# Optimization experiments

Hardware: AMD Instinct MI355X
Metric: run time of the kernel (lower is better)

Reference implementation:

```python
import jax, jax.numpy as jnp
import numpy as np

N_NODES = 50000


def gcn_conv(x, edge_index, W, b):
    """PyG GCNConv: h = x @ W; add self-loops; symmetric deg^-1/2 norm; scatter-add; + bias."""
    h = x @ W                                   # [N, C_out]
    n = x.shape[0]
    loops = jnp.arange(n, dtype=edge_index.dtype)
    src = jnp.concatenate([edge_index[0], loops])   # [E + N]
    dst = jnp.concatenate([edge_index[1], loops])   # [E + N]
    deg = jax.ops.segment_sum(jnp.ones_like(src, dtype=h.dtype), dst, num_segments=n)
    dinv = jnp.where(deg > 0, jax.lax.rsqrt(deg), 0.0)
    norm = dinv[src] * dinv[dst]                # [E + N]
    msg = h[src] * norm[:, None]                # gather + edgewise scale
    out = jax.ops.segment_sum(msg, dst, num_segments=n)  # scatter-add
    return out + b


def setup_inputs() -> dict:
    key = jax.random.key(0)
    k1, k2, k3, k4 = jax.random.split(key, 4)
    x = jax.random.normal(k1, (N_NODES, 128), dtype=jnp.float32)
    edge_index = jax.random.randint(k2, (2, 800000), 0, N_NODES, dtype=jnp.int32)
    W1 = jax.random.normal(k3, (128, 128), dtype=jnp.float32) * (1.0 / np.sqrt(128))
    b1 = jnp.zeros((128,), dtype=jnp.float32)
    W2 = jax.random.normal(k4, (128, 64), dtype=jnp.float32) * (1.0 / np.sqrt(128))
    b2 = jnp.zeros((64,), dtype=jnp.float32)
    return {"x": x, "edge_index": edge_index, "W1": W1, "b1": b1, "W2": W2, "b2": b2}


def reference(x, edge_index, W1, b1, W2, b2):
    h = gcn_conv(x, edge_index, W1, b1)
    h = jax.nn.relu(h)
    out = gcn_conv(h, edge_index, W2, b2)
    return out
```

## Files before the change

kernel.cpp:

```cpp
#include <hip/hip_runtime.h>
#include <hip/hip_bf16.h>
#include <math.h>

#define N_NODES 50000
#define N_EDGES 800000
#define NSLICE 8
#define SLICE_NODES 6400
#define CSR_W 48
#define EDGE_CHUNKS ((N_EDGES + 1023) / 1024)
#define GROUPS 196

typedef unsigned int uint;
typedef unsigned short ushort;
typedef __attribute__((ext_vector_type(8))) short bf16x8;
typedef __attribute__((ext_vector_type(4))) float f32x4;

__device__ __forceinline__ float bf16_lo(uint u) { return __uint_as_float(u << 16); }
__device__ __forceinline__ float bf16_hi(uint u) { return __uint_as_float(u & 0xFFFF0000u); }
__device__ __forceinline__ ushort f2bf(float a) {
    return __bfloat16_as_ushort(__float2bfloat16(a));
}
__device__ __forceinline__ uint pack_bf2(float a, float b) {
    return ((uint)f2bf(b) << 16) | (uint)f2bf(a);
}

__global__ __launch_bounds__(256) void setup_kernel(const float* __restrict__ W1,
                                                    const float* __restrict__ W2,
                                                    int* __restrict__ counts,
                                                    ushort* __restrict__ W1t,
                                                    ushort* __restrict__ W2t,
                                                    ushort* __restrict__ h1pad,
                                                    ushort* __restrict__ h2pad) {
    int i = blockIdx.x * 256 + threadIdx.x;
    if (i < N_NODES + 1) { counts[i] = 0; return; }
    i -= N_NODES + 1;
    if (i < 128 * 128) {
        int k = i >> 7, n = i & 127;
        W1t[n * 128 + k] = f2bf(W1[i]);
        return;
    }
    i -= 128 * 128;
    if (i < 128 * 64) {
        int k = i >> 6, n = i & 63;
        W2t[n * 128 + k] = f2bf(W2[i]);
        return;
    }
    i -= 128 * 64;
    if (i < 128) { h1pad[i] = 0; return; }
    i -= 128;
    if (i < 64) h2pad[i] = 0;
}

__global__ __launch_bounds__(256) void fused_gemm1_build(const int* __restrict__ ei,
                                                         int* __restrict__ counts,
                                                         int* __restrict__ csr,
                                                         const float* __restrict__ X,
                                                         const ushort* __restrict__ W1t,
                                                         ushort* __restrict__ H) {
    int grp = blockIdx.x / 40;
    int r = blockIdx.x % 40;
    if (r < 32) {
        int b = grp * 32 + r;
        int slice = b & (NSLICE - 1);
        int chunk = b / NSLICE;
        int lo = slice * SLICE_NODES;
        int hi = lo + SLICE_NODES;
        int base = chunk * 1024 + threadIdx.x * 4;
        if (base + 3 < N_EDGES) {
            int4 d = *reinterpret_cast<const int4*>(ei + N_EDGES + base);
            int4 s = *reinterpret_cast<const int4*>(ei + base);
            if (d.x >= lo && d.x < hi) {
                int rr = atomicAdd(&counts[d.x], 1);
                if (rr < CSR_W) csr[d.x * CSR_W + rr] = s.x;
            }
            if (d.y >= lo && d.y < hi) {
                int rr = atomicAdd(&counts[d.y], 1);
                if (rr < CSR_W) csr[d.y * CSR_W + rr] = s.y;
            }
            if (d.z >= lo && d.z < hi) {
                int rr = atomicAdd(&counts[d.z], 1);
                if (rr < CSR_W) csr[d.z * CSR_W + rr] = s.z;
            }
            if (d.w >= lo && d.w < hi) {
                int rr = atomicAdd(&counts[d.w], 1);
                if (rr < CSR_W) csr[d.w * CSR_W + rr] = s.w;
            }
        }
        return;
    }
    int bid = grp * 8 + (r - 32);
    int lane = threadIdx.x & 63;
    int w = threadIdx.x >> 6;
    int m = lane & 15;
    int q = lane >> 4;
    int rowTile = bid * 2 + (w >> 1);
    int nbase = (w & 1) * 64;
    if (rowTile >= N_NODES / 16) return;

    const float* arow = X + (size_t)(rowTile * 16 + m) * 128 + q * 8;
    bf16x8 afrag[4];
#pragma unroll
    for (int kt = 0; kt < 4; kt++) {
        float4 lo4 = *reinterpret_cast<const float4*>(arow + kt * 32);
        float4 hi4 = *reinterpret_cast<const float4*>(arow + kt * 32 + 4);
        uint4 u;
        u.x = pack_bf2(lo4.x, lo4.y);
        u.y = pack_bf2(lo4.z, lo4.w);
        u.z = pack_bf2(hi4.x, hi4.y);
        u.w = pack_bf2(hi4.z, hi4.w);
        afrag[kt] = *reinterpret_cast<bf16x8*>(&u);
    }

    const ushort* brow = W1t + (size_t)(nbase + m) * 128 + q * 8;
    f32x4 acc[4];
#pragma unroll
    for (int nt = 0; nt < 4; nt++) {
        acc[nt] = {0.f, 0.f, 0.f, 0.f};
        const ushort* bp = brow + (size_t)nt * 16 * 128;
#pragma unroll
        for (int kt = 0; kt < 4; kt++) {
            bf16x8 bfrag = *reinterpret_cast<const bf16x8*>(bp + kt * 32);
            acc[nt] = __builtin_amdgcn_mfma_f32_16x16x32_bf16(afrag[kt], bfrag, acc[nt], 0, 0, 0);
        }
    }

    int rbase = rowTile * 16 + q * 4;
#pragma unroll
    for (int rr = 0; rr < 4; rr++) {
#pragma unroll
        for (int nt = 0; nt < 4; nt++) {
            H[(size_t)(rbase + rr) * 128 + nbase + nt * 16 + m] = f2bf(acc[nt][rr]);
        }
    }
}

__global__ __launch_bounds__(256) void agg1_gemm2_kernel(
    const __hip_bfloat16* __restrict__ Hb, const int* __restrict__ counts,
    const int* __restrict__ csr, const float* __restrict__ bias,
    const ushort* __restrict__ W2t, ushort* __restrict__ H2) {
    __shared__ uint4 g1lds[4][16];

    int wave = threadIdx.x >> 6;
    int lane = threadIdx.x & 63;
    int n = blockIdx.x * 4 + wave;

    int cntF = counts[n];
    float dn = rsqrtf((float)(cntF + 1));
    int cnt = (cntF < CSR_W) ? cntF : CSR_W;
    int my = (lane < cnt) ? csr[n * CSR_W + lane] : N_NODES;
    float mys = rsqrtf((float)(counts[my] + 1));

    int ql = lane & 15;
    int quarter = lane >> 4;
    float a[8];
    {
        uint4 u = reinterpret_cast<const uint4*>(Hb + (size_t)n * 128)[ql];
        float self = dn;
        a[0] = quarter ? 0.f : self * bf16_lo(u.x);
        a[1] = quarter ? 0.f : self * bf16_hi(u.x);
        a[2] = quarter ? 0.f : self * bf16_lo(u.y);
        a[3] = quarter ? 0.f : self * bf16_hi(u.y);
        a[4] = quarter ? 0.f : self * bf16_lo(u.z);
        a[5] = quarter ? 0.f : self * bf16_hi(u.z);
        a[6] = quarter ? 0.f : self * bf16_lo(u.w);
        a[7] = quarter ? 0.f : self * bf16_hi(u.w);
    }
    for (int j = 0; j < cnt; j += 32) {
        int rem = cnt - j;
        int s[8];
        float ds[8];
        uint4 v[8];
#pragma unroll
        for (int k = 0; k < 8; k++) {
            s[k] = __shfl(my, j + 4 * k + quarter, 64);
            ds[k] = __shfl(mys, j + 4 * k + quarter, 64);
        }
#pragma unroll
        for (int k = 0; k < 8; k++) {
            if (4 * k < rem)
                v[k] = reinterpret_cast<const uint4*>(Hb + (size_t)s[k] * 128)[ql];
            else
                v[k] = make_uint4(0, 0, 0, 0);
        }
#pragma unroll
        for (int k = 0; k < 8; k++) {
            a[0] = fmaf(ds[k], bf16_lo(v[k].x), a[0]);
            a[1] = fmaf(ds[k], bf16_hi(v[k].x), a[1]);
            a[2] = fmaf(ds[k], bf16_lo(v[k].y), a[2]);
            a[3] = fmaf(ds[k], bf16_hi(v[k].y), a[3]);
            a[4] = fmaf(ds[k], bf16_lo(v[k].z), a[4]);
            a[5] = fmaf(ds[k], bf16_hi(v[k].z), a[5]);
            a[6] = fmaf(ds[k], bf16_lo(v[k].w), a[6]);
            a[7] = fmaf(ds[k], bf16_hi(v[k].w), a[7]);
        }
    }
#pragma unroll
    for (int r = 0; r < 8; r++) {
        a[r] += __shfl_xor(a[r], 16, 64);
        a[r] += __shfl_xor(a[r], 32, 64);
    }
    if (quarter == 0) {
        float o[8];
#pragma unroll
        for (int r = 0; r < 8; r++) {
            o[r] = fmaxf(fmaf(a[r], dn, bias[8 * ql + r]), 0.f);
        }
        uint4 u;
        u.x = pack_bf2(o[0], o[1]);
        u.y = pack_bf2(o[2], o[3]);
        u.z = pack_bf2(o[4], o[5]);
        u.w = pack_bf2(o[6], o[7]);
        g1lds[wave][ql] = u;
    }
    __syncthreads();

    if (wave == 0) {
        int m = lane & 15;
        int q = lane >> 4;
        bf16x8 afrag[4];
#pragma unroll
        for (int kt = 0; kt < 4; kt++)
            afrag[kt] = *reinterpret_cast<const bf16x8*>(&g1lds[m & 3][kt * 4 + q]);

        const ushort* brow = W2t + (size_t)m * 128 + q * 8;
        f32x4 acc[4];
#pragma unroll
        for (int nt = 0; nt < 4; nt++) {
            acc[nt] = {0.f, 0.f, 0.f, 0.f};
            const ushort* bp = brow + (size_t)nt * 16 * 128;
#pragma unroll
            for (int kt = 0; kt < 4; kt++) {
                bf16x8 bfrag = *reinterpret_cast<const bf16x8*>(bp + kt * 32);
                acc[nt] = __builtin_amdgcn_mfma_f32_16x16x32_bf16(afrag[kt], bfrag, acc[nt], 0, 0, 0);
            }
        }
        if (q == 0) {
            int n0 = blockIdx.x * 4;
#pragma unroll
            for (int r = 0; r < 4; r++) {
                float dn2 = rsqrtf((float)(counts[n0 + r] + 1));
#pragma unroll
                for (int nt = 0; nt < 4; nt++) {
                    H2[(size_t)(n0 + r) * 64 + nt * 16 + m] = f2bf(acc[nt][r] * dn2);
                }
            }
        }
    }
}

__global__ __launch_bounds__(256) void agg2_kernel(const __hip_bfloat16* __restrict__ Hb,
                                                   const int* __restrict__ counts,
                                                   const int* __restrict__ csr,
                                                   const float* __restrict__ bias,
                                                   float* __restrict__ OUT) {
    int wave = threadIdx.x >> 6;
    int lane = threadIdx.x & 63;
    int n = blockIdx.x * 4 + wave;
    if (n >= N_NODES) return;

    int cntF = counts[n];
    float dn = rsqrtf((float)(cntF + 1));
    int cnt = (cntF < CSR_W) ? cntF : CSR_W;
    int my = (lane < cnt) ? csr[n * CSR_W + lane] : N_NODES;

    int gl = lane & 7;
    int group = lane >> 3;
    float a[8];
    {
        uint4 u = reinterpret_cast<const uint4*>(Hb + (size_t)n * 64)[gl];
        a[0] = group ? 0.f : bf16_lo(u.x);
        a[1] = group ? 0.f : bf16_hi(u.x);
        a[2] = group ? 0.f : bf16_lo(u.y);
        a[3] = group ? 0.f : bf16_hi(u.y);
        a[4] = group ? 0.f : bf16_lo(u.z);
        a[5] = group ? 0.f : bf16_hi(u.z);
        a[6] = group ? 0.f : bf16_lo(u.w);
        a[7] = group ? 0.f : bf16_hi(u.w);
    }
    {
        int s[8];
        uint4 v[8];
#pragma unroll
        for (int k = 0; k < 8; k++) s[k] = __shfl(my, 8 * k + group, 64);
#pragma unroll
        for (int k = 0; k < 8; k++) {
            if (8 * k < cnt)
                v[k] = reinterpret_cast<const uint4*>(Hb + (size_t)s[k] * 64)[gl];
            else
                v[k] = make_uint4(0, 0, 0, 0);
        }
#pragma unroll
        for (int k = 0; k < 8; k++) {
            a[0] += bf16_lo(v[k].x);
            a[1] += bf16_hi(v[k].x);
            a[2] += bf16_lo(v[k].y);
            a[3] += bf16_hi(v[k].y);
            a[4] += bf16_lo(v[k].z);
            a[5] += bf16_hi(v[k].z);
            a[6] += bf16_lo(v[k].w);
            a[7] += bf16_hi(v[k].w);
        }
    }
#pragma unroll
    for (int r = 0; r < 8; r++) {
        a[r] += __shfl_xor(a[r], 8, 64);
        a[r] += __shfl_xor(a[r], 16, 64);
        a[r] += __shfl_xor(a[r], 32, 64);
    }
    if (group == 0) {
        float o[8];
#pragma unroll
        for (int r = 0; r < 8; r++) o[r] = fmaf(a[r], dn, bias[8 * gl + r]);
        reinterpret_cast<float4*>(OUT)[(size_t)n * 16 + 2 * gl] =
            make_float4(o[0], o[1], o[2], o[3]);
        reinterpret_cast<float4*>(OUT)[(size_t)n * 16 + 2 * gl + 1] =
            make_float4(o[4], o[5], o[6], o[7]);
    }
}

extern "C" void kernel_launch(void* const* d_in, const int* in_sizes, int n_in,
                              void* d_out, int out_size, void* d_ws, size_t ws_size,
                              hipStream_t stream) {
    const float* x  = (const float*)d_in[0];
    const int*   ei = (const int*)d_in[1];
    const float* W1 = (const float*)d_in[2];
    const float* b1 = (const float*)d_in[3];
    const float* W2 = (const float*)d_in[4];
    const float* b2 = (const float*)d_in[5];
    float* out = (float*)d_out;

    char* ws = (char*)d_ws;
    auto alloc = [&](size_t bytes) -> char* {
        char* p = ws;
        ws += (bytes + 255) / 256 * 256;
        return p;
    };
    int* counts = (int*)alloc((size_t)(N_NODES + 1) * 4);
    int* csr = (int*)alloc((size_t)N_NODES * CSR_W * 4);
    ushort* W1t = (ushort*)alloc((size_t)128 * 128 * 2);
    ushort* W2t = (ushort*)alloc((size_t)64 * 128 * 2);
    ushort* h1 = (ushort*)alloc((size_t)(N_NODES + 1) * 128 * 2);
    ushort* h2 = (ushort*)alloc((size_t)(N_NODES + 1) * 64 * 2);

    const int SETUP_N = (N_NODES + 1) + 128 * 128 + 128 * 64 + 128 + 64;
    setup_kernel<<<(SETUP_N + 255) / 256, 256, 0, stream>>>(
        W1, W2, counts, W1t, W2t, h1 + (size_t)N_NODES * 128, h2 + (size_t)N_NODES * 64);
    fused_gemm1_build<<<GROUPS * 40, 256, 0, stream>>>(ei, counts, csr, x, W1t, h1);
    agg1_gemm2_kernel<<<N_NODES / 4, 256, 0, stream>>>(
        (const __hip_bfloat16*)h1, counts, csr, b1, W2t, h2);
    agg2_kernel<<<(N_NODES + 3) / 4, 256, 0, stream>>>(
        (const __hip_bfloat16*)h2, counts, csr, b2, out);
}
```

Baseline: 128.3 us.

## Split agg1+gemm2 into staged kernels interleaving second-half aggregation with first-half GEMM

Removes the per-block LDS handoff and __syncthreads, where only one of four waves ran the 4-row MFMA GEMM. Layer-1 aggregation now writes a full G1 buffer, and the second GEMM runs as full 16-row MFMA tiles. Those GEMM tiles for the first half of nodes are interleaved inside the kernel that aggregates the second half, and a tail kernel finishes the rest. In exchange it adds a 12.8MB intermediate write and read plus two extra kernel launches.

```diff
diff --git a/kernel.cpp b/kernel.cpp
--- a/kernel.cpp
+++ b/kernel.cpp
@@ -9,6 +9,11 @@
 #define CSR_W 48
 #define EDGE_CHUNKS ((N_EDGES + 1023) / 1024)
 #define GROUPS 196
+#define N_HALF 25600
+#define AGG1_H1_BLOCKS 6400
+#define AGG1_H2_BLOCKS 6100
+#define GEMM2_H1_BLOCKS 400
+#define INTER_GROUPS 407
 
 typedef unsigned int uint;
 typedef unsigned short ushort;
@@ -134,16 +139,12 @@
     }
 }
 
-__global__ __launch_bounds__(256) void agg1_gemm2_kernel(
-    const __hip_bfloat16* __restrict__ Hb, const int* __restrict__ counts,
-    const int* __restrict__ csr, const float* __restrict__ bias,
-    const ushort* __restrict__ W2t, ushort* __restrict__ H2) {
-    __shared__ uint4 g1lds[4][16];
-
-    int wave = threadIdx.x >> 6;
+__device__ __forceinline__ void agg1_body(int n, const __hip_bfloat16* __restrict__ Hb,
+                                          const int* __restrict__ counts,
+                                          const int* __restrict__ csr,
+                                          const float* __restrict__ bias,
+                                          ushort* __restrict__ G1) {
     int lane = threadIdx.x & 63;
-    int n = blockIdx.x * 4 + wave;
-
     int cntF = counts[n];
     float dn = rsqrtf((float)(cntF + 1));
     int cnt = (cntF < CSR_W) ? cntF : CSR_W;
@@ -155,15 +156,14 @@
     float a[8];
     {
         uint4 u = reinterpret_cast<const uint4*>(Hb + (size_t)n * 128)[ql];
-        float self = dn;
-        a[0] = quarter ? 0.f : self * bf16_lo(u.x);
-        a[1] = quarter ? 0.f : self * bf16_hi(u.x);
-        a[2] = quarter ? 0.f : self * bf16_lo(u.y);
-        a[3] = quarter ? 0.f : self * bf16_hi(u.y);
-        a[4] = quarter ? 0.f : self * bf16_lo(u.z);
-        a[5] = quarter ? 0.f : self * bf16_hi(u.z);
-        a[6] = quarter ? 0.f : self * bf16_lo(u.w);
-        a[7] = quarter ? 0.f : self * bf16_hi(u.w);
+        a[0] = quarter ? 0.f : dn * bf16_lo(u.x);
+        a[1] = quarter ? 0.f : dn * bf16_hi(u.x);
+        a[2] = quarter ? 0.f : dn * bf16_lo(u.y);
+        a[3] = quarter ? 0.f : dn * bf16_hi(u.y);
+        a[4] = quarter ? 0.f : dn * bf16_lo(u.z);
+        a[5] = quarter ? 0.f : dn * bf16_hi(u.z);
+        a[6] = quarter ? 0.f : dn * bf16_lo(u.w);
+        a[7] = quarter ? 0.f : dn * bf16_hi(u.w);
     }
     for (int j = 0; j < cnt; j += 32) {
         int rem = cnt - j;
@@ -202,50 +202,92 @@
     if (quarter == 0) {
         float o[8];
 #pragma unroll
-        for (int r = 0; r < 8; r++) {
+        for (int r = 0; r < 8; r++)
             o[r] = fmaxf(fmaf(a[r], dn, bias[8 * ql + r]), 0.f);
-        }
         uint4 u;
         u.x = pack_bf2(o[0], o[1]);
         u.y = pack_bf2(o[2], o[3]);
         u.z = pack_bf2(o[4], o[5]);
         u.w = pack_bf2(o[6], o[7]);
-        g1lds[wave][ql] = u;
-    }
-    __syncthreads();
-
-    if (wave == 0) {
-        int m = lane & 15;
-        int q = lane >> 4;
-        bf16x8 afrag[4];
-#pragma unroll
-        for (int kt = 0; kt < 4; kt++)
-            afrag[kt] = *reinterpret_cast<const bf16x8*>(&g1lds[m & 3][kt * 4 + q]);
-
-        const ushort* brow = W2t + (size_t)m * 128 + q * 8;
-        f32x4 acc[4];
+        reinterpret_cast<uint4*>(G1)[(size_t)n * 16 + ql] = u;
+    }
+}
+
+__device__ __forceinline__ void gemm2_body(int rowTile, const ushort* __restrict__ Ain,
+                                           const ushort* __restrict__ Wt,
+                                           const int* __restrict__ counts,
+                                           ushort* __restrict__ H) {
+    if (rowTile >= N_NODES / 16) return;
+    int lane = threadIdx.x & 63;
+    int m = lane & 15;
+    int q = lane >> 4;
+
+    const ushort* arow = Ain + (size_t)(rowTile * 16 + m) * 128 + q * 8;
+    bf16x8 afrag[4];
+#pragma unroll
+    for (int kt = 0; kt < 4; kt++)
+        afrag[kt] = *reinterpret_cast<const bf16x8*>(arow + kt * 32);
+
+    const ushort* brow = Wt + (size_t)m * 128 + q * 8;
+    f32x4 acc[4];
+#pragma unroll
+    for (int nt = 0; nt < 4; nt++) {
+        acc[nt] = {0.f, 0.f, 0.f, 0.f};
+        const ushort* bp = brow + (size_t)nt * 16 * 128;
+#pragma unroll
+        for (int kt = 0; kt < 4; kt++) {
+            bf16x8 bfrag = *reinterpret_cast<const bf16x8*>(bp + kt * 32);
+            acc[nt] = __builtin_amdgcn_mfma_f32_16x16x32_bf16(afrag[kt], bfrag, acc[nt], 0, 0, 0);
+        }
+    }
+
+    int rbase = rowTile * 16 + q * 4;
+#pragma unroll
+    for (int r = 0; r < 4; r++) {
+        float dn = rsqrtf((float)(counts[rbase + r] + 1));
 #pragma unroll
         for (int nt = 0; nt < 4; nt++) {
-            acc[nt] = {0.f, 0.f, 0.f, 0.f};
-            const ushort* bp = brow + (size_t)nt * 16 * 128;
-#pragma unroll
-            for (int kt = 0; kt < 4; kt++) {
-                bf16x8 bfrag = *reinterpret_cast<const bf16x8*>(bp + kt * 32);
-                acc[nt] = __builtin_amdgcn_mfma_f32_16x16x32_bf16(afrag[kt], bfrag, acc[nt], 0, 0, 0);
-            }
-        }
-        if (q == 0) {
-            int n0 = blockIdx.x * 4;
-#pragma unroll
-            for (int r = 0; r < 4; r++) {
-                float dn2 = rsqrtf((float)(counts[n0 + r] + 1));
-#pragma unroll
-                for (int nt = 0; nt < 4; nt++) {
-                    H2[(size_t)(n0 + r) * 64 + nt * 16 + m] = f2bf(acc[nt][r] * dn2);
-                }
-            }
-        }
-    }
+            H[(size_t)(rbase + r) * 64 + nt * 16 + m] = f2bf(acc[nt][r] * dn);
+        }
+    }
+}
+
+__global__ __launch_bounds__(256) void agg1_h1_kernel(const __hip_bfloat16* __restrict__ Hb,
+                                                      const int* __restrict__ counts,
+                                                      const int* __restrict__ csr,
+                                                      const float* __restrict__ b1,
+                                                      ushort* __restrict__ G1) {
+    int n = blockIdx.x * 4 + (threadIdx.x >> 6);
+    agg1_body(n, Hb, counts, csr, b1, G1);
+}
+
+__global__ __launch_bounds__(256) void agg1_gemm2_inter(const __hip_bfloat16* __restrict__ Hb,
+                                                        const int* __restrict__ counts,
+                                                        const int* __restrict__ csr,
+                                                        const float* __restrict__ b1,
+                                                        ushort* __restrict__ G1,
+                                                        const ushort* __restrict__ W2t,
+                                                        ushort* __restrict__ H2) {
+    int grp = blockIdx.x >> 4;
+    int r = blockIdx.x & 15;
+    if (r < 15) {
+        int bid = grp * 15 + r;
+        if (bid >= AGG1_H2_BLOCKS) return;
+        int n = N_HALF + bid * 4 + (threadIdx.x >> 6);
+        agg1_body(n, Hb, counts, csr, b1, G1);
+    } else {
+        if (grp >= GEMM2_H1_BLOCKS) return;
+        int w = threadIdx.x >> 6;
+        gemm2_body(grp * 4 + w, G1, W2t, counts, H2);
+    }
+}
+
+__global__ __launch_bounds__(256) void gemm2_tail_kernel(const ushort* __restrict__ G1,
+                                                         const ushort* __restrict__ W2t,
+                                                         const int* __restrict__ counts,
+                                                         ushort* __restrict__ H2) {
+    int w = threadIdx.x >> 6;
+    gemm2_body(N_HALF / 16 + blockIdx.x * 4 + w, G1, W2t, counts, H2);
 }
 
 __global__ __launch_bounds__(256) void agg2_kernel(const __hip_bfloat16* __restrict__ Hb,
@@ -340,14 +382,19 @@
     ushort* W1t = (ushort*)alloc((size_t)128 * 128 * 2);
     ushort* W2t = (ushort*)alloc((size_t)64 * 128 * 2);
     ushort* h1 = (ushort*)alloc((size_t)(N_NODES + 1) * 128 * 2);
+    ushort* g1 = (ushort*)alloc((size_t)N_NODES * 128 * 2);
     ushort* h2 = (ushort*)alloc((size_t)(N_NODES + 1) * 64 * 2);
 
     const int SETUP_N = (N_NODES + 1) + 128 * 128 + 128 * 64 + 128 + 64;
     setup_kernel<<<(SETUP_N + 255) / 256, 256, 0, stream>>>(
         W1, W2, counts, W1t, W2t, h1 + (size_t)N_NODES * 128, h2 + (size_t)N_NODES * 64);
     fused_gemm1_build<<<GROUPS * 40, 256, 0, stream>>>(ei, counts, csr, x, W1t, h1);
-    agg1_gemm2_kernel<<<N_NODES / 4, 256, 0, stream>>>(
-        (const __hip_bfloat16*)h1, counts, csr, b1, W2t, h2);
+    agg1_h1_kernel<<<AGG1_H1_BLOCKS, 256, 0, stream>>>(
+        (const __hip_bfloat16*)h1, counts, csr, b1, g1);
+    agg1_gemm2_inter<<<INTER_GROUPS * 16, 256, 0, stream>>>(
+        (const __hip_bfloat16*)h1, counts, csr, b1, g1, W2t, h2);
+    gemm2_tail_kernel<<<(N_NODES / 16 - N_HALF / 16 + 3) / 4, 256, 0, stream>>>(
+        g1, W2t, counts, h2);
     agg2_kernel<<<(N_NODES + 3) / 4, 256, 0, stream>>>(
         (const __hip_bfloat16*)h2, counts, csr, b2, out);
 }
```

New measurement: 164.5 us. 28.2% more time.
